# Kernel optimization log

Hardware: AMD Instinct MI355X
Metric: run time of the kernel (lower is better)

The kernel has to match this reference:

```python
import jax, jax.numpy as jnp
import numpy as np
import math

N, T, D, H = 64, 512, 512, 512

def setup_inputs() -> dict:
    key = jax.random.key(0)
    k1, k2, k3, k4 = jax.random.split(key, 4)
    x = jax.random.normal(k1, (N, T, D), dtype=jnp.float32)
    h0 = jax.random.normal(k2, (N, H), dtype=jnp.float32)
    Wx = jax.random.normal(k3, (D, 4 * H), dtype=jnp.float32) / math.sqrt(D)
    Wh = jax.random.normal(k4, (H, 4 * H), dtype=jnp.float32) / math.sqrt(H)
    b = jnp.zeros((4 * H,), dtype=jnp.float32)
    return {"x": x, "h0": h0, "Wx": Wx, "Wh": Wh, "b": b}

def reference(x, h0, Wx, Wh, b):
    # Precompute input projections for all timesteps as one big GEMM: [N,T,4H]
    xW = jnp.einsum('ntd,dk->ntk', x, Wx) + b
    c0 = jnp.zeros_like(h0)

    def step(carry, xw_t):
        h, c = carry
        gates = xw_t + h @ Wh          # [N,4H]
        i, f, o, g = jnp.split(gates, 4, axis=1)
        i = jax.nn.sigmoid(i)
        f = jax.nn.sigmoid(f)
        o = jax.nn.sigmoid(o)
        g = jnp.tanh(g)
        c = f * c + i * g
        h = o * jnp.tanh(c)
        return (h, c), h

    # scan over time: move T to leading axis
    (_, _), hs = jax.lax.scan(step, (h0, c0), jnp.swapaxes(xW, 0, 1))
    return jnp.swapaxes(hs, 0, 1)  # [N,T,H]
```

## Files before the change

kernel.cpp:

```cpp
#include <hip/hip_runtime.h>
#include <cstddef>


typedef _Float16 half8 __attribute__((ext_vector_type(8)));
typedef float f32x4 __attribute__((ext_vector_type(4)));

#define NBATCH 64
#define TSTEPS 512
#define DIN    512
#define HID    512
#define NCOL   2048
#define SCAN_WGS 128
#define LDK    536

__device__ __forceinline__ float fast_sigmoid(float x) {
  return 1.0f / (1.0f + __expf(-x));
}
__device__ __forceinline__ float fast_tanh(float x) {
  return 1.0f - 2.0f / (__expf(2.0f * x) + 1.0f);
}

__global__ void lstm_prep(const float* __restrict__ x, const float* __restrict__ h0,
                          _Float16* __restrict__ xb, _Float16* __restrict__ hbuf,
                          unsigned* __restrict__ flags)
{
  size_t gid = (size_t)blockIdx.x * blockDim.x + threadIdx.x;
  size_t stride = (size_t)gridDim.x * blockDim.x;
  const size_t NX = (size_t)NBATCH * TSTEPS * DIN;
  for (size_t i = gid * 4; i < NX; i += stride * 4) {
    float4 v = *(const float4*)(x + i);
    xb[i + 0] = (_Float16)v.x;
    xb[i + 1] = (_Float16)v.y;
    xb[i + 2] = (_Float16)v.z;
    xb[i + 3] = (_Float16)v.w;
  }
  for (size_t i = gid; i < (size_t)NBATCH * HID; i += stride)
    hbuf[i] = (_Float16)h0[i];
  if (gid < SCAN_WGS) flags[gid] = 0u;
}

__global__ __launch_bounds__(256, 1) void lstm_scan(
    const _Float16* __restrict__ xb,
    const float* __restrict__ Wx,
    const float* __restrict__ Wh,
    const float* __restrict__ bias,
    _Float16* __restrict__ hbuf,
    float* __restrict__ out,
    unsigned* __restrict__ flags)
{
  __shared__ _Float16 WxT[16][LDK];
  __shared__ _Float16 WhT[16][LDK];
  __shared__ float gl[NBATCH][17];
  __shared__ float cl[NBATCH][4];
  __shared__ float bl[16];

  const int wg   = blockIdx.x;
  const int tid  = threadIdx.x;
  const int lane = tid & 63;
  const int wave = tid >> 6;

  {
    const int gate = tid & 3;
    const int k0   = tid >> 2;
    for (int pass = 0; pass < 8; ++pass) {
      int k = k0 + pass * 64;
      float4 vx = *(const float4*)(Wx + (size_t)k * NCOL + gate * 512 + wg * 4);
      float4 vh = *(const float4*)(Wh + (size_t)k * NCOL + gate * 512 + wg * 4);
      WxT[gate * 4 + 0][k] = (_Float16)vx.x;
      WxT[gate * 4 + 1][k] = (_Float16)vx.y;
      WxT[gate * 4 + 2][k] = (_Float16)vx.z;
      WxT[gate * 4 + 3][k] = (_Float16)vx.w;
      WhT[gate * 4 + 0][k] = (_Float16)vh.x;
      WhT[gate * 4 + 1][k] = (_Float16)vh.y;
      WhT[gate * 4 + 2][k] = (_Float16)vh.z;
      WhT[gate * 4 + 3][k] = (_Float16)vh.w;
    }
    if (tid < 16) bl[tid] = bias[(tid >> 2) * 512 + wg * 4 + (tid & 3)];
    for (int i = tid; i < NBATCH * 4; i += 256) cl[i >> 2][i & 3] = 0.0f;
  }
  __syncthreads();

  const int fr = lane & 15;
  const int fk = (lane >> 4) * 8;
  const int mrow = wave * 16 + fr;
  const int n_ep = tid >> 2;
  const int hj_ep = tid & 3;
  const size_t out_col = (size_t)wg * 4 + hj_ep;

  half8 xa[16];
#pragma unroll
  for (int ks = 0; ks < 16; ++ks)
    xa[ks] = *(const half8*)(xb + ((size_t)mrow * TSTEPS + 0) * DIN + ks * 32 + fk);

  for (int t = 0; t < TSTEPS; ++t) {
    if (t > 0) {
      if (tid < 64) {
        const unsigned tgt = (unsigned)t;
        for (;;) {
          unsigned long long v = __hip_atomic_load(
              (const unsigned long long*)flags + tid,
              __ATOMIC_RELAXED, __HIP_MEMORY_SCOPE_AGENT);
          bool ok = ((unsigned)v >= tgt) && ((unsigned)(v >> 32) >= tgt);
          if (__all(ok)) break;
          __builtin_amdgcn_s_sleep(1);
        }
      }
      __syncthreads();
    }

    const _Float16* hsrc = hbuf + (size_t)(t & 1) * (NBATCH * HID) + (size_t)mrow * HID;
    half8 ha[16];
#pragma unroll
    for (int ks = 0; ks < 16; ++ks) {
      const _Float16* p = hsrc + ks * 32 + fk;
      asm volatile("global_load_dwordx4 %0, %1, off sc1"
                   : "=v"(ha[ks]) : "v"(p) : "memory");
    }

    f32x4 a0 = {0.f, 0.f, 0.f, 0.f};
    f32x4 a1 = {0.f, 0.f, 0.f, 0.f};
    f32x4 a2 = {0.f, 0.f, 0.f, 0.f};
    f32x4 a3 = {0.f, 0.f, 0.f, 0.f};
#pragma unroll
    for (int ks = 0; ks < 16; ks += 4) {
      half8 b0 = *(const half8*)(&WxT[fr][ks * 32 + fk]);
      half8 b1 = *(const half8*)(&WxT[fr][(ks + 1) * 32 + fk]);
      half8 b2 = *(const half8*)(&WxT[fr][(ks + 2) * 32 + fk]);
      half8 b3 = *(const half8*)(&WxT[fr][(ks + 3) * 32 + fk]);
      a0 = __builtin_amdgcn_mfma_f32_16x16x32_f16(xa[ks],     b0, a0, 0, 0, 0);
      a1 = __builtin_amdgcn_mfma_f32_16x16x32_f16(xa[ks + 1], b1, a1, 0, 0, 0);
      a2 = __builtin_amdgcn_mfma_f32_16x16x32_f16(xa[ks + 2], b2, a2, 0, 0, 0);
      a3 = __builtin_amdgcn_mfma_f32_16x16x32_f16(xa[ks + 3], b3, a3, 0, 0, 0);
    }

    asm volatile("s_waitcnt vmcnt(0)" ::: "memory");
    __builtin_amdgcn_sched_barrier(0);

#pragma unroll
    for (int ks = 0; ks < 16; ks += 4) {
      half8 b0 = *(const half8*)(&WhT[fr][ks * 32 + fk]);
      half8 b1 = *(const half8*)(&WhT[fr][(ks + 1) * 32 + fk]);
      half8 b2 = *(const half8*)(&WhT[fr][(ks + 2) * 32 + fk]);
      half8 b3 = *(const half8*)(&WhT[fr][(ks + 3) * 32 + fk]);
      a0 = __builtin_amdgcn_mfma_f32_16x16x32_f16(ha[ks],     b0, a0, 0, 0, 0);
      a1 = __builtin_amdgcn_mfma_f32_16x16x32_f16(ha[ks + 1], b1, a1, 0, 0, 0);
      a2 = __builtin_amdgcn_mfma_f32_16x16x32_f16(ha[ks + 2], b2, a2, 0, 0, 0);
      a3 = __builtin_amdgcn_mfma_f32_16x16x32_f16(ha[ks + 3], b3, a3, 0, 0, 0);
    }
    f32x4 acc = (a0 + a1) + (a2 + a3);

    {
      int gr = wave * 16 + ((lane >> 4) << 2);
#pragma unroll
      for (int j = 0; j < 4; ++j) gl[gr + j][fr] = acc[j];
    }
    __syncthreads();

    {
      float iv = gl[n_ep][0  + hj_ep] + bl[0  + hj_ep];
      float fv = gl[n_ep][4  + hj_ep] + bl[4  + hj_ep];
      float ov = gl[n_ep][8  + hj_ep] + bl[8  + hj_ep];
      float gv = gl[n_ep][12 + hj_ep] + bl[12 + hj_ep];
      float ig = fast_sigmoid(iv);
      float fg = fast_sigmoid(fv);
      float og = fast_sigmoid(ov);
      float gg = fast_tanh(gv);
      float c = fg * cl[n_ep][hj_ep] + ig * gg;
      cl[n_ep][hj_ep] = c;
      float hval = og * fast_tanh(c);
      out[((size_t)n_ep * TSTEPS + t) * HID + out_col] = hval;

      float hpart = __shfl_xor(hval, 1);
      if ((hj_ep & 1) == 0) {
        _Float16 lo = (_Float16)hval, hi = (_Float16)hpart;
        unsigned packed = (unsigned)__builtin_bit_cast(unsigned short, lo) |
                          ((unsigned)__builtin_bit_cast(unsigned short, hi) << 16);
        unsigned* dst = (unsigned*)(hbuf + (size_t)((t + 1) & 1) * (NBATCH * HID) +
                                    (size_t)n_ep * HID + wg * 4 + hj_ep);
        __hip_atomic_store(dst, packed, __ATOMIC_RELAXED, __HIP_MEMORY_SCOPE_AGENT);
      }
    }

    asm volatile("s_waitcnt vmcnt(0)" ::: "memory");
    __syncthreads();
    if (tid == 0)
      __hip_atomic_store(&flags[wg], (unsigned)(t + 1),
                         __ATOMIC_RELAXED, __HIP_MEMORY_SCOPE_AGENT);

    if (t + 1 < TSTEPS) {
#pragma unroll
      for (int ks = 0; ks < 16; ++ks)
        xa[ks] = *(const half8*)(xb + ((size_t)mrow * TSTEPS + (t + 1)) * DIN + ks * 32 + fk);
    }
  }
}

extern "C" void kernel_launch(void* const* d_in, const int* in_sizes, int n_in,
                              void* d_out, int out_size, void* d_ws, size_t ws_size,
                              hipStream_t stream) {
  const float* x  = (const float*)d_in[0];
  const float* h0 = (const float*)d_in[1];
  const float* Wx = (const float*)d_in[2];
  const float* Wh = (const float*)d_in[3];
  const float* b  = (const float*)d_in[4];
  float* out = (float*)d_out;

  char* ws = (char*)d_ws;
  _Float16* xb    = (_Float16*)ws;
  _Float16* hbuf  = (_Float16*)(ws + 33554432);
  unsigned* flags = (unsigned*)(ws + 33554432 + 131072);

  lstm_prep<<<dim3(2048), dim3(256), 0, stream>>>(x, h0, xb, hbuf, flags);
  lstm_scan<<<dim3(SCAN_WGS), dim3(256), 0, stream>>>(xb, Wx, Wh, b, hbuf, out, flags);
}
```

Baseline: 2.720 ms.

## Store weights in MFMA fragment layout and use cache invalidate for h loads

Weights in LDS are repacked into a fragment-major layout, so each lane reads its MFMA B operand as one contiguous half8 indexed by lane, with simpler addressing and possibly fewer bank conflicts. The per-load sc1 hidden-state loads are replaced by a single buffer_inv sc1 after the flag barrier followed by ordinary loads, which may let the compiler schedule them more freely. The output store becomes an inline sc1 store. The explicit wait between the Wx and Wh MFMA phases is removed, so the compiler now decides where to wait on the h loads.

```diff
diff --git a/kernel.cpp b/kernel.cpp
--- a/kernel.cpp
+++ b/kernel.cpp
@@ -11,7 +11,6 @@
 #define HID    512
 #define NCOL   2048
 #define SCAN_WGS 128
-#define LDK    536
 
 __device__ __forceinline__ float fast_sigmoid(float x) {
   return 1.0f / (1.0f + __expf(-x));
@@ -48,8 +47,8 @@
     float* __restrict__ out,
     unsigned* __restrict__ flags)
 {
-  __shared__ _Float16 WxT[16][LDK];
-  __shared__ _Float16 WhT[16][LDK];
+  __shared__ half8 WxF[16][64];
+  __shared__ half8 WhF[16][64];
   __shared__ float gl[NBATCH][17];
   __shared__ float cl[NBATCH][4];
   __shared__ float bl[16];
@@ -62,18 +61,21 @@
   {
     const int gate = tid & 3;
     const int k0   = tid >> 2;
+    _Float16* wx = (_Float16*)WxF;
+    _Float16* wh = (_Float16*)WhF;
     for (int pass = 0; pass < 8; ++pass) {
       int k = k0 + pass * 64;
       float4 vx = *(const float4*)(Wx + (size_t)k * NCOL + gate * 512 + wg * 4);
       float4 vh = *(const float4*)(Wh + (size_t)k * NCOL + gate * 512 + wg * 4);
-      WxT[gate * 4 + 0][k] = (_Float16)vx.x;
-      WxT[gate * 4 + 1][k] = (_Float16)vx.y;
-      WxT[gate * 4 + 2][k] = (_Float16)vx.z;
-      WxT[gate * 4 + 3][k] = (_Float16)vx.w;
-      WhT[gate * 4 + 0][k] = (_Float16)vh.x;
-      WhT[gate * 4 + 1][k] = (_Float16)vh.y;
-      WhT[gate * 4 + 2][k] = (_Float16)vh.z;
-      WhT[gate * 4 + 3][k] = (_Float16)vh.w;
+      int base = (k >> 5) * 512 + (((k >> 3) & 3) * 16 + gate * 4) * 8 + (k & 7);
+      wx[base + 0 * 8] = (_Float16)vx.x;
+      wx[base + 1 * 8] = (_Float16)vx.y;
+      wx[base + 2 * 8] = (_Float16)vx.z;
+      wx[base + 3 * 8] = (_Float16)vx.w;
+      wh[base + 0 * 8] = (_Float16)vh.x;
+      wh[base + 1 * 8] = (_Float16)vh.y;
+      wh[base + 2 * 8] = (_Float16)vh.z;
+      wh[base + 3 * 8] = (_Float16)vh.w;
     }
     if (tid < 16) bl[tid] = bias[(tid >> 2) * 512 + wg * 4 + (tid & 3)];
     for (int i = tid; i < NBATCH * 4; i += 256) cl[i >> 2][i & 3] = 0.0f;
@@ -106,16 +108,15 @@
         }
       }
       __syncthreads();
+      asm volatile("s_waitcnt vmcnt(0)\n\tbuffer_inv sc1" ::: "memory");
+      __builtin_amdgcn_sched_barrier(0);
     }
 
     const _Float16* hsrc = hbuf + (size_t)(t & 1) * (NBATCH * HID) + (size_t)mrow * HID;
     half8 ha[16];
 #pragma unroll
-    for (int ks = 0; ks < 16; ++ks) {
-      const _Float16* p = hsrc + ks * 32 + fk;
-      asm volatile("global_load_dwordx4 %0, %1, off sc1"
-                   : "=v"(ha[ks]) : "v"(p) : "memory");
-    }
+    for (int ks = 0; ks < 16; ++ks)
+      ha[ks] = *(const half8*)(hsrc + ks * 32 + fk);
 
     f32x4 a0 = {0.f, 0.f, 0.f, 0.f};
     f32x4 a1 = {0.f, 0.f, 0.f, 0.f};
@@ -123,29 +124,17 @@
     f32x4 a3 = {0.f, 0.f, 0.f, 0.f};
 #pragma unroll
     for (int ks = 0; ks < 16; ks += 4) {
-      half8 b0 = *(const half8*)(&WxT[fr][ks * 32 + fk]);
-      half8 b1 = *(const half8*)(&WxT[fr][(ks + 1) * 32 + fk]);
-      half8 b2 = *(const half8*)(&WxT[fr][(ks + 2) * 32 + fk]);
-      half8 b3 = *(const half8*)(&WxT[fr][(ks + 3) * 32 + fk]);
-      a0 = __builtin_amdgcn_mfma_f32_16x16x32_f16(xa[ks],     b0, a0, 0, 0, 0);
-      a1 = __builtin_amdgcn_mfma_f32_16x16x32_f16(xa[ks + 1], b1, a1, 0, 0, 0);
-      a2 = __builtin_amdgcn_mfma_f32_16x16x32_f16(xa[ks + 2], b2, a2, 0, 0, 0);
-      a3 = __builtin_amdgcn_mfma_f32_16x16x32_f16(xa[ks + 3], b3, a3, 0, 0, 0);
-    }
-
-    asm volatile("s_waitcnt vmcnt(0)" ::: "memory");
-    __builtin_amdgcn_sched_barrier(0);
-
+      a0 = __builtin_amdgcn_mfma_f32_16x16x32_f16(xa[ks],     WxF[ks][lane],     a0, 0, 0, 0);
+      a1 = __builtin_amdgcn_mfma_f32_16x16x32_f16(xa[ks + 1], WxF[ks + 1][lane], a1, 0, 0, 0);
+      a2 = __builtin_amdgcn_mfma_f32_16x16x32_f16(xa[ks + 2], WxF[ks + 2][lane], a2, 0, 0, 0);
+      a3 = __builtin_amdgcn_mfma_f32_16x16x32_f16(xa[ks + 3], WxF[ks + 3][lane], a3, 0, 0, 0);
+    }
 #pragma unroll
     for (int ks = 0; ks < 16; ks += 4) {
-      half8 b0 = *(const half8*)(&WhT[fr][ks * 32 + fk]);
-      half8 b1 = *(const half8*)(&WhT[fr][(ks + 1) * 32 + fk]);
-      half8 b2 = *(const half8*)(&WhT[fr][(ks + 2) * 32 + fk]);
-      half8 b3 = *(const half8*)(&WhT[fr][(ks + 3) * 32 + fk]);
-      a0 = __builtin_amdgcn_mfma_f32_16x16x32_f16(ha[ks],     b0, a0, 0, 0, 0);
-      a1 = __builtin_amdgcn_mfma_f32_16x16x32_f16(ha[ks + 1], b1, a1, 0, 0, 0);
-      a2 = __builtin_amdgcn_mfma_f32_16x16x32_f16(ha[ks + 2], b2, a2, 0, 0, 0);
-      a3 = __builtin_amdgcn_mfma_f32_16x16x32_f16(ha[ks + 3], b3, a3, 0, 0, 0);
+      a0 = __builtin_amdgcn_mfma_f32_16x16x32_f16(ha[ks],     WhF[ks][lane],     a0, 0, 0, 0);
+      a1 = __builtin_amdgcn_mfma_f32_16x16x32_f16(ha[ks + 1], WhF[ks + 1][lane], a1, 0, 0, 0);
+      a2 = __builtin_amdgcn_mfma_f32_16x16x32_f16(ha[ks + 2], WhF[ks + 2][lane], a2, 0, 0, 0);
+      a3 = __builtin_amdgcn_mfma_f32_16x16x32_f16(ha[ks + 3], WhF[ks + 3][lane], a3, 0, 0, 0);
     }
     f32x4 acc = (a0 + a1) + (a2 + a3);
 
@@ -168,7 +157,10 @@
       float c = fg * cl[n_ep][hj_ep] + ig * gg;
       cl[n_ep][hj_ep] = c;
       float hval = og * fast_tanh(c);
-      out[((size_t)n_ep * TSTEPS + t) * HID + out_col] = hval;
+
+      const float* outp = out + ((size_t)n_ep * TSTEPS + t) * HID + out_col;
+      asm volatile("global_store_dword %0, %1, off sc1"
+                   :: "v"(outp), "v"(hval) : "memory");
 
       float hpart = __shfl_xor(hval, 1);
       if ((hj_ep & 1) == 0) {
```

Measured after the change: 3.915 ms. +44.0%, slower.
